# Optimization experiments

Measured on AMD Instinct MI355X. Metric: run time of the kernel, lower is better.

The kernel has to match this reference:

```python
import jax, jax.numpy as jnp
import numpy as np

COMMITMENT_COST = 0.25
NUM_EMBEDDINGS = 512
EMBEDDING_DIM = 64


def setup_inputs() -> dict:
    key = jax.random.key(0)
    k1, k2 = jax.random.split(key)
    inputs = jax.random.normal(k1, (64, EMBEDDING_DIM, 32, 32), dtype=jnp.float32)
    # nn.Embedding init: uniform(-1/K, 1/K)
    emb_w = jax.random.uniform(
        k2, (NUM_EMBEDDINGS, EMBEDDING_DIM), dtype=jnp.float32,
        minval=-1.0 / NUM_EMBEDDINGS, maxval=1.0 / NUM_EMBEDDINGS)
    return {"inputs": inputs, "emb_w": emb_w}


def reference(inputs, emb_w):
    sg = jax.lax.stop_gradient
    # NCHW -> NHWC
    x = jnp.transpose(inputs, (0, 2, 3, 1))          # [B, H, W, D]
    B, H, W, D = x.shape
    flat = x.reshape(-1, D)                          # [N, D]
    dist = (jnp.sum(flat * flat, axis=1, keepdims=True)
            + jnp.sum(emb_w * emb_w, axis=1)
            - 2.0 * jnp.dot(flat, emb_w.T))          # [N, K]
    idx = jnp.argmin(dist, axis=1)                   # [N]
    # one-hot @ emb_w is just a gather
    quantized = emb_w[idx].reshape(B, H, W, D)       # [B, H, W, D]
    e_latent_loss = jnp.mean((sg(quantized) - x) ** 2)
    q_latent_loss = jnp.mean((quantized - sg(x)) ** 2)
    loss = q_latent_loss + COMMITMENT_COST * e_latent_loss
    # straight-through estimator
    quantized_st = x + sg(quantized - x)
    out = jnp.transpose(quantized_st, (0, 3, 1, 2))  # back to NCHW
    return loss, out, idx[:, None]
```

## Files before the change

kernel.cpp:

```cpp
#include <hip/hip_runtime.h>


#define D_    64
#define HW_   1024
#define N_    65536
#define K_    512
#define NDTOT 4194304
#define PB_   64
#define KW_   128

__global__ __launch_bounds__(256) void vq_norm_kernel(const float* __restrict__ emb,
                                                      float* __restrict__ wsn) {
    int k = blockIdx.x * 256 + threadIdx.x;
    if (k < K_) {
        const float* e = emb + k * D_;
        float r[8];
#pragma unroll
        for (int j = 0; j < 8; ++j) r[j] = __fmul_rn(e[j], e[j]);
#pragma unroll
        for (int i = 1; i < 8; ++i)
#pragma unroll
            for (int j = 0; j < 8; ++j)
                r[j] = __fadd_rn(r[j], __fmul_rn(e[i * 8 + j], e[i * 8 + j]));
        wsn[k] = __fadd_rn(__fadd_rn(__fadd_rn(r[0], r[1]), __fadd_rn(r[2], r[3])),
                           __fadd_rn(__fadd_rn(r[4], r[5]), __fadd_rn(r[6], r[7])));
    }
}

__global__ __launch_bounds__(256, 4) void vq_main_kernel(const float* __restrict__ inp,
                                                         const float* __restrict__ emb,
                                                         const float* __restrict__ wsn,
                                                         float* __restrict__ out) {
    __shared__ float sv[4][PB_];
    __shared__ int   si[4][PB_];
    __shared__ int   fi[PB_];

    const int tid  = threadIdx.x;
    const int lane = tid & 63;
    const int wv   = __builtin_amdgcn_readfirstlane(tid >> 6);

    const int n0  = blockIdx.x * PB_;
    const int b   = n0 >> 10;
    const int hw0 = n0 & 1023;
    const float* xcol = inp + b * (D_ * HW_) + hw0 + lane;

    float x[64];
#pragma unroll
    for (int d = 0; d < D_; ++d) x[d] = xcol[d * HW_];

    float r[8];
#pragma unroll
    for (int j = 0; j < 8; ++j) r[j] = __fmul_rn(x[j], x[j]);
#pragma unroll
    for (int i = 1; i < 8; ++i)
#pragma unroll
        for (int j = 0; j < 8; ++j)
            r[j] = __fadd_rn(r[j], __fmul_rn(x[i * 8 + j], x[i * 8 + j]));
    const float sx = __fadd_rn(__fadd_rn(__fadd_rn(r[0], r[1]), __fadd_rn(r[2], r[3])),
                               __fadd_rn(__fadd_rn(r[4], r[5]), __fadd_rn(r[6], r[7])));

    float runv = 3.4e38f;
    int   runi = 0;
    const int k0 = wv * KW_;
    for (int kk = 0; kk < KW_; ++kk) {
        const int k = k0 + kk;
        const float* e = emb + k * D_;
        float acc = 0.f;
#pragma unroll
        for (int d = 0; d < D_; ++d)
            acc = fmaf(x[d], e[d], acc);
        float t1 = __fadd_rn(sx, wsn[k]);
        float v  = fmaf(-2.0f, acc, t1);
        if (v < runv) { runv = v; runi = k; }
    }
    sv[wv][lane] = runv;
    si[wv][lane] = runi;
    __syncthreads();

    if (tid < PB_) {
        float bv = 3.4e38f; int bi = 0;
#pragma unroll
        for (int g = 0; g < 4; ++g) {
            float v  = sv[g][tid];
            int   ii = si[g][tid];
            if (v < bv) { bv = v; bi = ii; }
        }
        fi[tid] = bi;
        out[1 + NDTOT + n0 + tid] = (float)bi;
    }
    __syncthreads();

    if (wv == 0) {
        const int idx = fi[lane];
        const float4* erow = (const float4*)(emb + idx * D_);
        float* ob = out + 1 + b * (D_ * HW_) + hw0 + lane;
        float local = 0.f;
#pragma unroll
        for (int j = 0; j < 16; ++j) {
            float4 e4 = erow[j];
            float ev[4] = {e4.x, e4.y, e4.z, e4.w};
#pragma unroll
            for (int c = 0; c < 4; ++c) {
                float df = ev[c] - x[j * 4 + c];
                local = fmaf(df, df, local);
                ob[(j * 4 + c) * HW_] = ev[c];
            }
        }
#pragma unroll
        for (int off = 32; off > 0; off >>= 1)
            local += __shfl_down(local, off, 64);
        if (lane == 0)
            atomicAdd(out, local * (1.25f / (float)NDTOT));
    }
}

extern "C" void kernel_launch(void* const* d_in, const int* in_sizes, int n_in,
                              void* d_out, int out_size, void* d_ws, size_t ws_size,
                              hipStream_t stream) {
    const float* inp = (const float*)d_in[0];
    const float* emb = (const float*)d_in[1];
    float* out = (float*)d_out;
    float* wsn = (float*)d_ws;

    hipMemsetAsync(d_out, 0, sizeof(float), stream);
    vq_norm_kernel<<<2, 256, 0, stream>>>(emb, wsn);
    vq_main_kernel<<<N_ / PB_, 256, 0, stream>>>(inp, emb, wsn, out);
}
```

Baseline: 151.0 us.

## Stage codebook chunks in LDS and interleave two codes per wave iteration

The codebook is now loaded into shared memory in four 128-code chunks, with block-wide syncs around each load. Each wave scans 32 codes per chunk from LDS, computing two dot products per iteration for more instruction-level parallelism. Previously every wave read its codes straight from global memory (scalar/broadcast loads). An empty asm barrier pins the x loads, and the final cross-wave reduction now breaks ties toward the lower index. The change adds 33KB of LDS per block, which may cut occupancy, and adds sync overhead.

```diff
diff --git a/kernel.cpp b/kernel.cpp
--- a/kernel.cpp
+++ b/kernel.cpp
@@ -7,7 +7,6 @@
 #define K_    512
 #define NDTOT 4194304
 #define PB_   64
-#define KW_   128
 
 __global__ __launch_bounds__(256) void vq_norm_kernel(const float* __restrict__ emb,
                                                       float* __restrict__ wsn) {
@@ -31,6 +30,8 @@
                                                          const float* __restrict__ emb,
                                                          const float* __restrict__ wsn,
                                                          float* __restrict__ out) {
+    __shared__ float ldse[128 * D_];
+    __shared__ float ldsn[128];
     __shared__ float sv[4][PB_];
     __shared__ int   si[4][PB_];
     __shared__ int   fi[PB_];
@@ -46,7 +47,11 @@
 
     float x[64];
 #pragma unroll
-    for (int d = 0; d < D_; ++d) x[d] = xcol[d * HW_];
+    for (int d = 0; d < D_; ++d) {
+        float v = xcol[d * HW_];
+        asm volatile("" : "+v"(v));
+        x[d] = v;
+    }
 
     float r[8];
 #pragma unroll
@@ -61,29 +66,49 @@
 
     float runv = 3.4e38f;
     int   runi = 0;
-    const int k0 = wv * KW_;
-    for (int kk = 0; kk < KW_; ++kk) {
-        const int k = k0 + kk;
-        const float* e = emb + k * D_;
-        float acc = 0.f;
+
+    for (int c = 0; c < 4; ++c) {
+        __syncthreads();
+        {
+            const float4* src = (const float4*)(emb + c * 128 * D_);
+            float4* dst = (float4*)ldse;
 #pragma unroll
-        for (int d = 0; d < D_; ++d)
-            acc = fmaf(x[d], e[d], acc);
-        float t1 = __fadd_rn(sx, wsn[k]);
-        float v  = fmaf(-2.0f, acc, t1);
-        if (v < runv) { runv = v; runi = k; }
+            for (int i = 0; i < 8; ++i) dst[i * 256 + tid] = src[i * 256 + tid];
+            if (tid < 128) ldsn[tid] = wsn[c * 128 + tid];
+        }
+        __syncthreads();
+
+        const float* ebase = ldse + wv * 32 * D_;
+        const int    kbase = c * 128 + wv * 32;
+        for (int j = 0; j < 32; j += 2) {
+            const float* e0 = ebase + j * D_;
+            const float* e1 = e0 + D_;
+            float a0 = 0.f, a1 = 0.f;
+#pragma unroll
+            for (int d = 0; d < D_; ++d) {
+                a0 = fmaf(x[d], e0[d], a0);
+                a1 = fmaf(x[d], e1[d], a1);
+            }
+            float nk0 = ldsn[wv * 32 + j];
+            float nk1 = ldsn[wv * 32 + j + 1];
+            float v0 = fmaf(-2.0f, a0, __fadd_rn(sx, nk0));
+            float v1 = fmaf(-2.0f, a1, __fadd_rn(sx, nk1));
+            if (v0 < runv) { runv = v0; runi = kbase + j; }
+            if (v1 < runv) { runv = v1; runi = kbase + j + 1; }
+        }
     }
+
     sv[wv][lane] = runv;
     si[wv][lane] = runi;
     __syncthreads();
 
     if (tid < PB_) {
-        float bv = 3.4e38f; int bi = 0;
+        float bv = 3.4e38f; int bi = 0x7fffffff;
 #pragma unroll
         for (int g = 0; g < 4; ++g) {
             float v  = sv[g][tid];
             int   ii = si[g][tid];
-            if (v < bv) { bv = v; bi = ii; }
+            if (v < bv || (v == bv && ii < bi)) { bv = v; bi = ii; }
         }
         fi[tid] = bi;
         out[1 + NDTOT + n0 + tid] = (float)bi;
@@ -100,10 +125,10 @@
             float4 e4 = erow[j];
             float ev[4] = {e4.x, e4.y, e4.z, e4.w};
 #pragma unroll
-            for (int c = 0; c < 4; ++c) {
-                float df = ev[c] - x[j * 4 + c];
+            for (int cc = 0; cc < 4; ++cc) {
+                float df = ev[cc] - x[j * 4 + cc];
                 local = fmaf(df, df, local);
-                ob[(j * 4 + c) * HW_] = ev[c];
+                ob[(j * 4 + cc) * HW_] = ev[cc];
             }
         }
 #pragma unroll
```

Result: slower. 158.0 us (+4.6%).
